# Kernel tuning notes

Measured on AMD Instinct MI355X. Metric: run time of the kernel, lower is better.

Reference implementation:

```python
import jax, jax.numpy as jnp
import numpy as np

N_NODES = 100000
N_EDGES = 1600000
IN_CH = 1024
FEAT_CH = 128
OUT_CH = 3


def setup_inputs() -> dict:
    key = jax.random.key(0)
    ks = jax.random.split(key, 9)
    features = jax.random.normal(ks[0], (N_NODES, IN_CH), dtype=jnp.float32)
    edges = jax.random.randint(ks[1], (2, N_EDGES), 0, N_NODES, dtype=jnp.int64)
    edges2 = jax.random.randint(ks[2], (2, N_EDGES), 0, N_NODES, dtype=jnp.int64)
    edge_features = jax.random.normal(ks[3], (N_EDGES, 1), dtype=jnp.float32)
    additional_feature = jax.random.normal(ks[4], (N_NODES, 20), dtype=jnp.float32)
    # GCNConv linear weights (glorot-ish scale) and biases
    W1 = jax.random.normal(ks[5], (IN_CH, FEAT_CH), dtype=jnp.float32) * (1.0 / np.sqrt(IN_CH))
    b1 = jnp.zeros((FEAT_CH,), dtype=jnp.float32)
    W2 = jax.random.normal(ks[6], (FEAT_CH, OUT_CH), dtype=jnp.float32) * (1.0 / np.sqrt(FEAT_CH))
    b2 = jnp.zeros((OUT_CH,), dtype=jnp.float32)
    return {"features": features, "edges": edges, "edges2": edges2,
            "edge_features": edge_features, "additional_feature": additional_feature,
            "W1": W1, "b1": b1, "W2": W2, "b2": b2}


def gcn_conv(x, edge_index, W, b, num_nodes):
    """PyG GCNConv: x' = D^{-1/2}(A+I)D^{-1/2} x W + b (self-loops added)."""
    x = x @ W  # project first (cheaper feature dim for aggregation)
    loop = jnp.arange(num_nodes, dtype=edge_index.dtype)
    src = jnp.concatenate([edge_index[0], loop])
    dst = jnp.concatenate([edge_index[1], loop])
    deg = jax.ops.segment_sum(jnp.ones_like(dst, dtype=x.dtype), dst,
                              num_segments=num_nodes)  # >=1 due to self-loops
    dinv = jax.lax.rsqrt(deg)
    norm = dinv[src] * dinv[dst]  # [E+N]
    out = jax.ops.segment_sum(x[src] * norm[:, None], dst, num_segments=num_nodes)
    return out + b


def reference(features, edges, edges2, edge_features, additional_feature, W1, b1, W2, b2):
    # use_additional_channels=False -> features unchanged; edge_features forced to None
    n = features.shape[0]
    x = gcn_conv(features, edges2, W1, b1, n)
    x = jax.nn.relu(x)
    # dropout inactive in eval mode
    return gcn_conv(x, edges2, W2, b2, n)
```

## Files before the change

kernel.cpp:

```cpp
#include <hip/hip_runtime.h>
#include <hip/hip_bf16.h>

typedef __attribute__((ext_vector_type(8))) _Float16 half8;
typedef __attribute__((ext_vector_type(4))) float f32x4;

#define N_NODES 100000
#define N_EDGES 1600000
#define IN_CH 1024
#define FEAT 128
#define CAP 64
#define NDIG 196
#define CAPC 10240
#define NTILES ((N_NODES + 127) / 128)

__global__ void k_prep(const float* __restrict__ W1, _Float16* __restrict__ W1t,
                       int* __restrict__ cursorC, int* __restrict__ done) {
    int idx = blockIdx.x * 256 + threadIdx.x;
    if (idx < IN_CH * FEAT) {
        int col = idx & (FEAT - 1), k = idx >> 7;
        W1t[(size_t)col * IN_CH + k] = (_Float16)W1[idx];
    }
    if (idx < NDIG) cursorC[idx] = idx * CAPC;
    if (idx == 0) *done = 0;
}

__global__ __launch_bounds__(256, 3) void k_build_gemm(
    const float* __restrict__ A, const _Float16* __restrict__ Bt,
    const int4* __restrict__ src4, const int4* __restrict__ dst4,
    int* __restrict__ cursorC, uint2* __restrict__ recs,
    int* __restrict__ csr, int* __restrict__ cnt, float* __restrict__ dinvarr,
    int* __restrict__ done, _Float16* __restrict__ H, int M, int e4)
{
    __shared__ union {
        _Float16 Bs[2][128][72];
        struct { int hist[NDIG], segoff[NDIG], lcur[NDIG]; } bin;
        int cl[512];
    } sm;
    const int t = threadIdx.x;

    if (blockIdx.x < NDIG) {
        const int b = blockIdx.x;
        if (t < NDIG) sm.bin.hist[t] = 0;
        __syncthreads();
        const int base4 = b * 2048;
        int4 sv[8], dv[8];
#pragma unroll
        for (int j = 0; j < 8; ++j) {
            int idx = base4 + j * 256 + t;
            if (idx < e4) { sv[j] = src4[idx]; dv[j] = dst4[idx]; }
            else { sv[j] = (int4){-1,-1,-1,-1}; dv[j] = (int4){-1,-1,-1,-1}; }
        }
#pragma unroll
        for (int j = 0; j < 8; ++j) {
            int dd[4] = {dv[j].x, dv[j].y, dv[j].z, dv[j].w};
            int ss[4] = {sv[j].x, sv[j].y, sv[j].z, sv[j].w};
#pragma unroll
            for (int c = 0; c < 4; ++c)
                if ((unsigned)dd[c] < N_NODES && (unsigned)ss[c] < N_NODES)
                    atomicAdd(&sm.bin.hist[dd[c] >> 9], 1);
        }
        __syncthreads();
        if (t < NDIG) {
            sm.bin.segoff[t] = atomicAdd(&cursorC[t], sm.bin.hist[t]);
            sm.bin.lcur[t] = 0;
        }
        __syncthreads();
#pragma unroll
        for (int j = 0; j < 8; ++j) {
            int dd[4] = {dv[j].x, dv[j].y, dv[j].z, dv[j].w};
            int ss[4] = {sv[j].x, sv[j].y, sv[j].z, sv[j].w};
#pragma unroll
            for (int c = 0; c < 4; ++c) {
                if ((unsigned)dd[c] < N_NODES && (unsigned)ss[c] < N_NODES) {
                    int dg = dd[c] >> 9;
                    int r = atomicAdd(&sm.bin.lcur[dg], 1);
                    int pos = sm.bin.segoff[dg] + r;
                    if (pos < (dg + 1) * CAPC)
                        recs[pos] = (uint2){(unsigned)ss[c], (unsigned)dd[c]};
                }
            }
        }
        __syncthreads();
        if (t == 0) {
            __threadfence();
            __hip_atomic_fetch_add(done, 1, __ATOMIC_RELEASE, __HIP_MEMORY_SCOPE_AGENT);
            while (__hip_atomic_load(done, __ATOMIC_ACQUIRE, __HIP_MEMORY_SCOPE_AGENT) < NDIG)
                __builtin_amdgcn_s_sleep(8);
        }
        __syncthreads();
        const int d = blockIdx.x;
        for (int j = t; j < 512; j += 256) sm.cl[j] = 0;
        __syncthreads();
        const int base = d * CAPC;
        int n = cursorC[d] - base;
        if (n > CAPC) n = CAPC;
        for (int k = t; k < n; k += 256) {
            uint2 r = recs[base + k];
            int local = (int)r.y & 511;
            int slot = atomicAdd(&sm.cl[local], 1);
            if (slot < CAP) csr[((int)r.y << 6) + slot] = (int)r.x;
        }
        __syncthreads();
        const int node0 = d << 9;
        for (int j = t; j < 512; j += 256) {
            int node = node0 + j;
            if (node < N_NODES) {
                int c = sm.cl[j] < CAP ? sm.cl[j] : CAP;
                cnt[node] = c;
                dinvarr[node] = rsqrtf((float)(c + 1));
            }
        }
        return;
    }

    const int wid = t >> 6, lane = t & 63;
    const int brow0 = (blockIdx.x - NDIG) * 128;
    const int NKT = IN_CH / 64;

    f32x4 acc[2][8];
#pragma unroll
    for (int m = 0; m < 2; ++m)
#pragma unroll
        for (int nn = 0; nn < 8; ++nn) acc[m][nn] = (f32x4){0.f, 0.f, 0.f, 0.f};

    int r0 = brow0 + wid * 32 + (lane & 15);
    int r1 = r0 + 16;
    if (r0 >= M) r0 = M - 1;
    if (r1 >= M) r1 = M - 1;
    const int kbase = (lane >> 4) * 8;
    const float* pa0 = A + (size_t)r0 * IN_CH + kbase;
    const float* pa1 = A + (size_t)r1 * IN_CH + kbase;
    const int bcol = t >> 1;
    const int bko = (t & 1) * 32;
    const _Float16* pb = Bt + (size_t)bcol * IN_CH + bko;

    float4 ar[2][2][2];
    half8 af[2][2];
    half8 bst[4];

#define LOAD_A(kt)                                                              \
    {                                                                           \
        _Pragma("unroll") for (int m = 0; m < 2; ++m) {                         \
            const float* p_ = (m ? pa1 : pa0) + (kt) * 64;                      \
            _Pragma("unroll") for (int kk = 0; kk < 2; ++kk) {                  \
                ar[m][kk][0] = *(const float4*)(p_ + kk * 32);                  \
                ar[m][kk][1] = *(const float4*)(p_ + kk * 32 + 4);              \
            }                                                                   \
        }                                                                       \
    }
#define CVT_A()                                                                 \
    {                                                                           \
        _Pragma("unroll") for (int m = 0; m < 2; ++m)                           \
        _Pragma("unroll") for (int kk = 0; kk < 2; ++kk) {                      \
            half8 h;                                                            \
            h[0] = (_Float16)ar[m][kk][0].x; h[1] = (_Float16)ar[m][kk][0].y;   \
            h[2] = (_Float16)ar[m][kk][0].z; h[3] = (_Float16)ar[m][kk][0].w;   \
            h[4] = (_Float16)ar[m][kk][1].x; h[5] = (_Float16)ar[m][kk][1].y;   \
            h[6] = (_Float16)ar[m][kk][1].z; h[7] = (_Float16)ar[m][kk][1].w;   \
            af[m][kk] = h;                                                      \
        }                                                                       \
    }
#define LOAD_B(kt)                                                              \
    {                                                                           \
        const half8* s_ = (const half8*)(pb + (kt) * 64);                       \
        _Pragma("unroll") for (int j = 0; j < 4; ++j) bst[j] = s_[j];           \
    }
#define WRITE_B(buf)                                                            \
    {                                                                           \
        _Pragma("unroll") for (int j = 0; j < 4; ++j)                           \
            *(half8*)(&sm.Bs[buf][bcol][bko + j * 8]) = bst[j];                 \
    }

    LOAD_A(0); LOAD_B(0);
    CVT_A();
    WRITE_B(0);
    __syncthreads();

    for (int kt = 0; kt < NKT; ++kt) {
        const int cur = kt & 1;
        const bool more = (kt + 1 < NKT);
        if (more) { LOAD_B(kt + 1); LOAD_A(kt + 1); }
#pragma unroll
        for (int kk = 0; kk < 2; ++kk) {
            half8 a0 = af[0][kk], a1 = af[1][kk];
#pragma unroll
            for (int nn = 0; nn < 8; ++nn) {
                half8 bb = *(const half8*)(&sm.Bs[cur][nn * 16 + (lane & 15)][kk * 32 + kbase]);
                acc[0][nn] = __builtin_amdgcn_mfma_f32_16x16x32_f16(a0, bb, acc[0][nn], 0, 0, 0);
                acc[1][nn] = __builtin_amdgcn_mfma_f32_16x16x32_f16(a1, bb, acc[1][nn], 0, 0, 0);
            }
        }
        if (more) {
            CVT_A();
            WRITE_B(cur ^ 1);
            __syncthreads();
        }
    }
#undef LOAD_A
#undef CVT_A
#undef LOAD_B
#undef WRITE_B

    int colb = lane & 15, rgrp = (lane >> 4) * 4;
#pragma unroll
    for (int m = 0; m < 2; ++m) {
#pragma unroll
        for (int r = 0; r < 4; ++r) {
            int grow = brow0 + wid * 32 + m * 16 + rgrp + r;
            if (grow < M) {
                _Float16* hp = H + (size_t)grow * FEAT + colb;
#pragma unroll
                for (int nn = 0; nn < 8; ++nn) hp[nn * 16] = (_Float16)acc[m][nn][r];
            }
        }
    }
}

__global__ __launch_bounds__(256) void k_agg1(const _Float16* __restrict__ H,
                                              const int* __restrict__ csr,
                                              const int* __restrict__ cnt,
                                              const float* __restrict__ dinvarr,
                                              const float* __restrict__ b1,
                                              const float* __restrict__ W2,
                                              float* __restrict__ Y, int n) {
    int wid = threadIdx.x >> 6, lane = threadIdx.x & 63;
    int i = blockIdx.x * 4 + wid;
    if (i >= n) return;
    const int g = lane >> 4, u = lane & 15;
    int m = cnt[i];
    float di = dinvarr[i];

    int sl; float dl;
    if (lane < m) { sl = csr[(i << 6) + lane]; dl = dinvarr[sl]; }
    else          { sl = i;                    dl = (lane == m) ? di : 0.f; }
    int mm = (m < 63 ? m : 63) + 1;

    float ax[8];
#pragma unroll
    for (int j = 0; j < 8; ++j) ax[j] = 0.f;

    for (int e = 0; e < mm; e += 16) {
        int idx0 = e + g, idx1 = e + 4 + g, idx2 = e + 8 + g, idx3 = e + 12 + g;
        bool v0 = idx0 < mm, v1 = idx1 < mm, v2 = idx2 < mm, v3 = idx3 < mm;
        int c0i = v0 ? idx0 : 0, c1i = v1 ? idx1 : 0;
        int c2i = v2 ? idx2 : 0, c3i = v3 ? idx3 : 0;
        int s0 = __shfl(sl, c0i); float w0 = __shfl(dl, c0i);
        int s1 = __shfl(sl, c1i); float w1 = __shfl(dl, c1i);
        int s2 = __shfl(sl, c2i); float w2 = __shfl(dl, c2i);
        int s3 = __shfl(sl, c3i); float w3 = __shfl(dl, c3i);
        if (!v0) { s0 = i; w0 = 0.f; }
        if (!v1) { s1 = i; w1 = 0.f; }
        if (!v2) { s2 = i; w2 = 0.f; }
        if (!v3) { s3 = i; w3 = 0.f; }
        half8 h0 = *(const half8*)(H + ((size_t)s0 << 7) + u * 8);
        half8 h1 = *(const half8*)(H + ((size_t)s1 << 7) + u * 8);
        half8 h2 = *(const half8*)(H + ((size_t)s2 << 7) + u * 8);
        half8 h3 = *(const half8*)(H + ((size_t)s3 << 7) + u * 8);
#pragma unroll
        for (int j = 0; j < 8; ++j)
            ax[j] += w0 * (float)h0[j] + w1 * (float)h1[j]
                   + w2 * (float)h2[j] + w3 * (float)h3[j];
    }

#pragma unroll
    for (int j = 0; j < 8; ++j) {
        ax[j] += __shfl_xor(ax[j], 16);
        ax[j] += __shfl_xor(ax[j], 32);
    }

    int c0 = u * 8;
    float y0 = 0.f, y1 = 0.f, y2 = 0.f;
#pragma unroll
    for (int j = 0; j < 8; ++j) {
        float x = di * ax[j] + b1[c0 + j];
        x = x > 0.f ? x : 0.f;
        y0 += x * W2[(c0 + j) * 3 + 0];
        y1 += x * W2[(c0 + j) * 3 + 1];
        y2 += x * W2[(c0 + j) * 3 + 2];
    }
#pragma unroll
    for (int d = 1; d < 16; d <<= 1) {
        y0 += __shfl_xor(y0, d);
        y1 += __shfl_xor(y1, d);
        y2 += __shfl_xor(y2, d);
    }
    if (lane == 0) {
        float* yp = Y + (size_t)i * 4;
        yp[0] = di * y0; yp[1] = di * y1; yp[2] = di * y2;
    }
}

__global__ void k_agg2(const float* __restrict__ Y, const int* __restrict__ csr,
                       const int* __restrict__ cnt, const float* __restrict__ dinvarr,
                       const float* __restrict__ b2, float* __restrict__ out, int n) {
    int i = blockIdx.x * 256 + threadIdx.x;
    if (i >= n) return;
    int m = cnt[i];
    float di = dinvarr[i];
    int base = i << 6;
    const float4* Y4 = (const float4*)Y;
    float4 self = Y4[i];
    float a0 = self.x, a1 = self.y, a2 = self.z;
    int e = 0;
    for (; e + 3 < m; e += 4) {
        int s0 = csr[base + e],     s1 = csr[base + e + 1];
        int s2 = csr[base + e + 2], s3 = csr[base + e + 3];
        float4 v0 = Y4[s0], v1 = Y4[s1], v2 = Y4[s2], v3 = Y4[s3];
        a0 += (v0.x + v1.x) + (v2.x + v3.x);
        a1 += (v0.y + v1.y) + (v2.y + v3.y);
        a2 += (v0.z + v1.z) + (v2.z + v3.z);
    }
    for (; e < m; ++e) {
        float4 v0 = Y4[csr[base + e]];
        a0 += v0.x; a1 += v0.y; a2 += v0.z;
    }
    out[(size_t)i * 3 + 0] = di * a0 + b2[0];
    out[(size_t)i * 3 + 1] = di * a1 + b2[1];
    out[(size_t)i * 3 + 2] = di * a2 + b2[2];
}

extern "C" void kernel_launch(void* const* d_in, const int* in_sizes, int n_in,
                              void* d_out, int out_size, void* d_ws, size_t ws_size,
                              hipStream_t stream) {
    const float* features = (const float*)d_in[0];
    const int* edges2 = (const int*)d_in[2];
    const float* W1 = (const float*)d_in[5];
    const float* b1 = (const float*)d_in[6];
    const float* W2 = (const float*)d_in[7];
    const float* b2 = (const float*)d_in[8];
    float* out = (float*)d_out;

    const int N = N_NODES, E = N_EDGES;
    const int4* src4 = (const int4*)edges2;
    const int4* dst4 = (const int4*)(edges2 + E);
    int e4 = E / 4;

    char* p = (char*)d_ws;
    auto carve = [&](size_t bytes) { char* q = p; p += (bytes + 255) & ~(size_t)255; return q; };
    int* cnt       = (int*)carve(4 * (size_t)N);
    float* dinvarr = (float*)carve(4 * (size_t)N);
    int* cursorC   = (int*)carve(4 * NDIG);
    int* done      = (int*)carve(4);
    uint2* recs    = (uint2*)carve(8 * (size_t)NDIG * CAPC);
    int* csr       = (int*)carve(4 * (size_t)N * CAP);
    _Float16* W1t  = (_Float16*)carve(2 * (size_t)IN_CH * FEAT);
    _Float16* H    = (_Float16*)carve(2 * (size_t)N * FEAT);
    float* Y       = (float*)carve(16 * (size_t)N);

    k_prep<<<dim3(512), dim3(256), 0, stream>>>(W1, W1t, cursorC, done);
    k_build_gemm<<<dim3(NDIG + NTILES), dim3(256), 0, stream>>>(
        features, W1t, src4, dst4, cursorC, recs, csr, cnt, dinvarr, done, H, N, e4);
    k_agg1<<<dim3((N + 3) / 4), dim3(256), 0, stream>>>(H, csr, cnt, dinvarr, b1, W2, Y, N);
    k_agg2<<<dim3((N + 255) / 256), dim3(256), 0, stream>>>(Y, csr, cnt, dinvarr, b2, out, N);
}
```

Baseline: 273.4 us.

## Stage A tile through swizzled LDS with coalesced loads in GEMM

The GEMM part of k_build_gemm now loads the fp32 A tile with a coalesced per-thread row mapping, converts it to fp16 and stores it in LDS alongside B. Both tiles use an XOR-swizzled 128-byte-row layout instead of padded rows. MFMA operands for A are read from LDS rather than taken straight from registers. This targets uncoalesced global reads of A and LDS bank conflicts, at the cost of more LDS traffic and footprint, so launch_bounds drops to 2 blocks per SM.

```diff
diff --git a/kernel.cpp b/kernel.cpp
--- a/kernel.cpp
+++ b/kernel.cpp
@@ -2,6 +2,7 @@
 #include <hip/hip_bf16.h>
 
 typedef __attribute__((ext_vector_type(8))) _Float16 half8;
+typedef __attribute__((ext_vector_type(4))) _Float16 half4;
 typedef __attribute__((ext_vector_type(4))) float f32x4;
 
 #define N_NODES 100000
@@ -13,6 +14,10 @@
 #define CAPC 10240
 #define NTILES ((N_NODES + 127) / 128)
 
+__device__ __forceinline__ int swz(int row, int colbyte) {
+    return row * 128 + (colbyte ^ ((row & 7) << 4));
+}
+
 __global__ void k_prep(const float* __restrict__ W1, _Float16* __restrict__ W1t,
                        int* __restrict__ cursorC, int* __restrict__ done) {
     int idx = blockIdx.x * 256 + threadIdx.x;
@@ -24,7 +29,7 @@
     if (idx == 0) *done = 0;
 }
 
-__global__ __launch_bounds__(256, 3) void k_build_gemm(
+__global__ __launch_bounds__(256, 2) void k_build_gemm(
     const float* __restrict__ A, const _Float16* __restrict__ Bt,
     const int4* __restrict__ src4, const int4* __restrict__ dst4,
     int* __restrict__ cursorC, uint2* __restrict__ recs,
@@ -32,7 +37,7 @@
     int* __restrict__ done, _Float16* __restrict__ H, int M, int e4)
 {
     __shared__ union {
-        _Float16 Bs[2][128][72];
+        struct { _Float16 As[2][128 * 64]; _Float16 Bsw[2][128 * 64]; } g;
         struct { int hist[NDIG], segoff[NDIG], lcur[NDIG]; } bin;
         int cl[512];
     } sm;
@@ -115,7 +120,6 @@
 
     const int wid = t >> 6, lane = t & 63;
     const int brow0 = (blockIdx.x - NDIG) * 128;
-    const int NKT = IN_CH / 64;
 
     f32x4 acc[2][8];
 #pragma unroll
@@ -123,83 +127,71 @@
 #pragma unroll
         for (int nn = 0; nn < 8; ++nn) acc[m][nn] = (f32x4){0.f, 0.f, 0.f, 0.f};
 
-    int r0 = brow0 + wid * 32 + (lane & 15);
-    int r1 = r0 + 16;
-    if (r0 >= M) r0 = M - 1;
-    if (r1 >= M) r1 = M - 1;
-    const int kbase = (lane >> 4) * 8;
-    const float* pa0 = A + (size_t)r0 * IN_CH + kbase;
-    const float* pa1 = A + (size_t)r1 * IN_CH + kbase;
+    const int sarow = t >> 4;
+    const int sacolB = (t & 15) * 8;
+    const float* paBase[8];
+#pragma unroll
+    for (int i = 0; i < 8; ++i) {
+        int grow = brow0 + i * 16 + sarow;
+        if (grow >= M) grow = M - 1;
+        paBase[i] = A + (size_t)grow * IN_CH + (t & 15) * 4;
+    }
     const int bcol = t >> 1;
-    const int bko = (t & 1) * 32;
-    const _Float16* pb = Bt + (size_t)bcol * IN_CH + bko;
-
-    float4 ar[2][2][2];
-    half8 af[2][2];
+    const int bhalf = (t & 1) * 64;
+    const _Float16* pb = Bt + (size_t)bcol * IN_CH + (t & 1) * 32;
+
+    float4 areg[8];
     half8 bst[4];
 
-#define LOAD_A(kt)                                                              \
+#define LOAD_AB(kt)                                                             \
     {                                                                           \
-        _Pragma("unroll") for (int m = 0; m < 2; ++m) {                         \
-            const float* p_ = (m ? pa1 : pa0) + (kt) * 64;                      \
-            _Pragma("unroll") for (int kk = 0; kk < 2; ++kk) {                  \
-                ar[m][kk][0] = *(const float4*)(p_ + kk * 32);                  \
-                ar[m][kk][1] = *(const float4*)(p_ + kk * 32 + 4);              \
+        _Pragma("unroll") for (int i = 0; i < 8; ++i)                           \
+            areg[i] = *(const float4*)(paBase[i] + (kt) * 64);                  \
+        const half8* s_ = (const half8*)(pb + (kt) * 64);                       \
+        _Pragma("unroll") for (int j = 0; j < 4; ++j) bst[j] = s_[j];           \
+    }
+#define CVT_WRITE(buf)                                                          \
+    {                                                                           \
+        _Pragma("unroll") for (int i = 0; i < 8; ++i) {                         \
+            half4 h;                                                            \
+            h[0] = (_Float16)areg[i].x; h[1] = (_Float16)areg[i].y;             \
+            h[2] = (_Float16)areg[i].z; h[3] = (_Float16)areg[i].w;             \
+            *(half4*)((char*)sm.g.As[buf] + swz(i * 16 + sarow, sacolB)) = h;   \
+        }                                                                       \
+        _Pragma("unroll") for (int j = 0; j < 4; ++j)                           \
+            *(half8*)((char*)sm.g.Bsw[buf] + swz(bcol, bhalf + j * 16)) = bst[j]; \
+    }
+#define MFMA_STEP(cur)                                                          \
+    {                                                                           \
+        _Pragma("unroll") for (int kk = 0; kk < 2; ++kk) {                      \
+            const int cb = kk * 64 + (lane >> 4) * 16;                          \
+            half8 a0 = *(const half8*)((char*)sm.g.As[cur] + swz(wid * 32 + (lane & 15), cb)); \
+            half8 a1 = *(const half8*)((char*)sm.g.As[cur] + swz(wid * 32 + 16 + (lane & 15), cb)); \
+            _Pragma("unroll") for (int nn = 0; nn < 8; ++nn) {                  \
+                half8 bb = *(const half8*)((char*)sm.g.Bsw[cur] + swz(nn * 16 + (lane & 15), cb)); \
+                acc[0][nn] = __builtin_amdgcn_mfma_f32_16x16x32_f16(a0, bb, acc[0][nn], 0, 0, 0); \
+                acc[1][nn] = __builtin_amdgcn_mfma_f32_16x16x32_f16(a1, bb, acc[1][nn], 0, 0, 0); \
             }                                                                   \
         }                                                                       \
     }
-#define CVT_A()                                                                 \
-    {                                                                           \
-        _Pragma("unroll") for (int m = 0; m < 2; ++m)                           \
-        _Pragma("unroll") for (int kk = 0; kk < 2; ++kk) {                      \
-            half8 h;                                                            \
-            h[0] = (_Float16)ar[m][kk][0].x; h[1] = (_Float16)ar[m][kk][0].y;   \
-            h[2] = (_Float16)ar[m][kk][0].z; h[3] = (_Float16)ar[m][kk][0].w;   \
-            h[4] = (_Float16)ar[m][kk][1].x; h[5] = (_Float16)ar[m][kk][1].y;   \
-            h[6] = (_Float16)ar[m][kk][1].z; h[7] = (_Float16)ar[m][kk][1].w;   \
-            af[m][kk] = h;                                                      \
-        }                                                                       \
-    }
-#define LOAD_B(kt)                                                              \
-    {                                                                           \
-        const half8* s_ = (const half8*)(pb + (kt) * 64);                       \
-        _Pragma("unroll") for (int j = 0; j < 4; ++j) bst[j] = s_[j];           \
-    }
-#define WRITE_B(buf)                                                            \
-    {                                                                           \
-        _Pragma("unroll") for (int j = 0; j < 4; ++j)                           \
-            *(half8*)(&sm.Bs[buf][bcol][bko + j * 8]) = bst[j];                 \
-    }
-
-    LOAD_A(0); LOAD_B(0);
-    CVT_A();
-    WRITE_B(0);
+
+    LOAD_AB(0);
+    CVT_WRITE(0);
     __syncthreads();
 
-    for (int kt = 0; kt < NKT; ++kt) {
+#pragma unroll 1
+    for (int kt = 0; kt < 16; ++kt) {
         const int cur = kt & 1;
-        const bool more = (kt + 1 < NKT);
-        if (more) { LOAD_B(kt + 1); LOAD_A(kt + 1); }
-#pragma unroll
-        for (int kk = 0; kk < 2; ++kk) {
-            half8 a0 = af[0][kk], a1 = af[1][kk];
-#pragma unroll
-            for (int nn = 0; nn < 8; ++nn) {
-                half8 bb = *(const half8*)(&sm.Bs[cur][nn * 16 + (lane & 15)][kk * 32 + kbase]);
-                acc[0][nn] = __builtin_amdgcn_mfma_f32_16x16x32_f16(a0, bb, acc[0][nn], 0, 0, 0);
-                acc[1][nn] = __builtin_amdgcn_mfma_f32_16x16x32_f16(a1, bb, acc[1][nn], 0, 0, 0);
-            }
-        }
-        if (more) {
-            CVT_A();
-            WRITE_B(cur ^ 1);
+        if (kt + 1 < 16) LOAD_AB(kt + 1);
+        MFMA_STEP(cur);
+        if (kt + 1 < 16) {
+            CVT_WRITE(cur ^ 1);
             __syncthreads();
         }
     }
-#undef LOAD_A
-#undef CVT_A
-#undef LOAD_B
-#undef WRITE_B
+#undef LOAD_AB
+#undef CVT_WRITE
+#undef MFMA_STEP
 
     int colb = lane & 15, rgrp = (lane >> 4) * 4;
 #pragma unroll
```

Result: faster. 252.6 us (-7.6%).
